# Optimization experiments

Hardware: AMD Instinct MI355X
Metric: run time of the kernel (lower is better)

The kernel has to match this reference:

```python
import jax, jax.numpy as jnp
import numpy as np

H, L, P, D_MODEL = 8, 4, 4, 256
HD = D_MODEL // H
SPATIAL = np.array([[100, 100], [50, 50], [25, 25], [13, 13]], dtype=np.int64)  # (h, w) per level


def _bilinear_sample(feat, gx, gy, lh, lw):
    """Bilinear sampling matching torch.F.grid_sample(align_corners=False, padding_mode='zeros').
    feat: [BH, lh*lw, D]; gx, gy: [BH, Nq, P] pixel coords. Returns [BH, Nq, P, D]."""
    x0 = jnp.floor(gx); y0 = jnp.floor(gy)
    wx = gx - x0; wy = gy - y0

    def gather(xf, yf):
        xi = xf.astype(jnp.int32); yi = yf.astype(jnp.int32)
        valid = (xi >= 0) & (xi < lw) & (yi >= 0) & (yi < lh)
        idx = jnp.clip(yi, 0, lh - 1) * lw + jnp.clip(xi, 0, lw - 1)
        BH = feat.shape[0]
        v = jnp.take_along_axis(feat, idx.reshape(BH, -1)[:, :, None], axis=1)
        v = v.reshape(xi.shape + (feat.shape[-1],))
        return v * valid[..., None].astype(feat.dtype)

    return (gather(x0, y0) * ((1 - wx) * (1 - wy))[..., None]
            + gather(x0 + 1, y0) * (wx * (1 - wy))[..., None]
            + gather(x0, y0 + 1) * ((1 - wx) * wy)[..., None]
            + gather(x0 + 1, y0 + 1) * (wx * wy)[..., None])


def _msda(query, reference_points, value, sp_np, Wso, bso, Waw, baw, Wv, bv, Wo, bo):
    B, Nq, _ = query.shape
    Nv = value.shape[1]
    v = (value @ Wv + bv).reshape(B, Nv, H, HD)  # value_proj
    off = (query @ Wso + bso).reshape(B, Nq, H, L, P, 2)  # sampling_offsets
    wh = jnp.asarray(sp_np[:, ::-1].copy(), jnp.float32)  # (w, h) per level
    loc = reference_points[:, :, None, :, None, :] + off / wh[None, None, None, :, None, :]
    grid = 2.0 * loc - 1.0  # [B, Nq, H, L, P, 2] in [-1, 1]
    aw = jax.nn.softmax((query @ Waw + baw).reshape(B, Nq, H, L * P), axis=-1).reshape(B, Nq, H, L, P)
    starts = np.concatenate([[0], np.cumsum(sp_np[:, 0] * sp_np[:, 1])]).astype(np.int64)
    out = jnp.zeros((B, H, Nq, HD), dtype=query.dtype)
    for lid in range(L):
        lh, lw = int(sp_np[lid, 0]), int(sp_np[lid, 1])
        feat = v[:, starts[lid]:starts[lid + 1]].transpose(0, 2, 1, 3).reshape(B * H, lh * lw, HD)
        g = grid[:, :, :, lid].transpose(0, 2, 1, 3, 4).reshape(B * H, Nq, P, 2)
        # align_corners=False: x_pix = ((gx + 1) * W - 1) / 2
        gx = (g[..., 0] + 1.0) * (lw * 0.5) - 0.5
        gy = (g[..., 1] + 1.0) * (lh * 0.5) - 0.5
        samp = _bilinear_sample(feat, gx, gy, lh, lw)  # [B*H, Nq, P, HD]
        w_l = aw[:, :, :, lid].transpose(0, 2, 1, 3).reshape(B * H, Nq, P)
        out = out + (samp * w_l[..., None]).sum(axis=2).reshape(B, H, Nq, HD)
    out = out.transpose(0, 2, 1, 3).reshape(B, Nq, D_MODEL)
    return out @ Wo + bo  # output_proj


def setup_inputs() -> dict:
    key = jax.random.key(0)
    ks = jax.random.split(key, 12)
    B, Nq = 2, int(np.sum(SPATIAL[:, 0] * SPATIAL[:, 1]))  # encoder: Nq == Nv == 13294
    Nv = Nq
    s = 1.0 / np.sqrt(D_MODEL).astype(np.float32)
    return {
        "query": jax.random.normal(ks[0], (B, Nq, D_MODEL), jnp.float32),
        "reference_points": jax.random.uniform(ks[1], (B, Nq, L, 2), dtype=jnp.float32),
        "value": jax.random.normal(ks[2], (B, Nv, D_MODEL), jnp.float32),
        "spatial_shapes": jnp.asarray(SPATIAL),
        "Wso": jax.random.normal(ks[3], (D_MODEL, H * L * P * 2), jnp.float32) * 0.01,
        "bso": jax.random.normal(ks[4], (H * L * P * 2,), jnp.float32) * 0.5,
        "Waw": jax.random.normal(ks[5], (D_MODEL, H * L * P), jnp.float32) * 0.01,
        "baw": jnp.zeros((H * L * P,), jnp.float32),
        "Wv": jax.random.normal(ks[6], (D_MODEL, D_MODEL), jnp.float32) * s,
        "bv": jnp.zeros((D_MODEL,), jnp.float32),
        "Wo": jax.random.normal(ks[7], (D_MODEL, D_MODEL), jnp.float32) * s,
        "bo": jnp.zeros((D_MODEL,), jnp.float32),
    }


def reference(query, reference_points, value, spatial_shapes, Wso, bso, Waw, baw, Wv, bv, Wo, bo):
    sp_np = np.asarray(spatial_shapes)  # static level shapes
    return _msda(query, reference_points, value, sp_np, Wso, bso, Waw, baw, Wv, bv, Wo, bo)
```

## Files before the change

kernel.cpp:

```cpp
#include <hip/hip_runtime.h>
#include <hip/hip_bf16.h>
#include <hip/hip_fp16.h>

typedef short s16x8 __attribute__((ext_vector_type(8)));
typedef float f32x4 __attribute__((ext_vector_type(4)));
typedef unsigned int u32x4 __attribute__((ext_vector_type(4)));
typedef unsigned int u32x2 __attribute__((ext_vector_type(2)));

constexpr int Bb = 2, NQ = 13294, Hh = 8, HD = 32;
constexpr int Mrows = Bb * NQ;

__device__ inline short bf16_of(float f) {
  __hip_bfloat16 h = __float2bfloat16(f);
  return *reinterpret_cast<short*>(&h);
}

__device__ __forceinline__ void gload16(const void* g, void* l) {
  __builtin_amdgcn_global_load_lds(
      (const __attribute__((address_space(1))) unsigned int*)g,
      (__attribute__((address_space(3))) unsigned int*)l, 16, 0, 0);
}

__global__ __launch_bounds__(256) void prep_k(
    const float* __restrict__ Wv, const float* __restrict__ Wso,
    const float* __restrict__ Waw, const float* __restrict__ Wo,
    const float* __restrict__ bso, const float* __restrict__ baw,
    short* __restrict__ WvT, short* __restrict__ WqT, short* __restrict__ WoT,
    float* __restrict__ bq)
{
  __shared__ short lds[64][65];
  const int tid = threadIdx.x;
  int t = blockIdx.x;
  if (t == 56) {
#pragma unroll
    for (int i = 0; i < 2; i++) {
      int id = i * 256 + tid;
      if (id < 384) bq[id] = id < 256 ? bso[id] : baw[id - 256];
    }
    return;
  }
  const float* src; short* dst; int ldS, n0, k0, drow0;
  if (t < 16)      { src = Wv;  dst = WvT; ldS = 256; n0 = (t >> 2) * 64;        k0 = (t & 3) * 64; drow0 = n0; }
  else if (t < 32) { t -= 16; src = Wso; dst = WqT; ldS = 256; n0 = (t >> 2) * 64; k0 = (t & 3) * 64; drow0 = n0; }
  else if (t < 40) { t -= 32; src = Waw; dst = WqT; ldS = 128; n0 = (t >> 2) * 64; k0 = (t & 3) * 64; drow0 = 256 + n0; }
  else             { t -= 40; src = Wo;  dst = WoT; ldS = 256; n0 = (t >> 2) * 64; k0 = (t & 3) * 64; drow0 = n0; }

#pragma unroll
  for (int i = 0; i < 16; i++) {
    int idx = i * 256 + tid;
    int kk = idx >> 6, nn = idx & 63;
    lds[nn][kk] = bf16_of(src[(size_t)(k0 + kk) * ldS + n0 + nn]);
  }
  __syncthreads();
#pragma unroll
  for (int i = 0; i < 16; i++) {
    int idx = i * 256 + tid;
    int nn = idx >> 6, kk = idx & 63;
    dst[(size_t)(drow0 + nn) * 256 + k0 + kk] = lds[nn][kk];
  }
}

template<int MODE>
__device__ __forceinline__ void gemm_body(
    const void* __restrict__ Araw, const short* __restrict__ WT,
    const float* __restrict__ bias, void* __restrict__ outraw,
    int wg, char* __restrict__ ldsA, char* __restrict__ ldsB)
{
  constexpr int NT = (MODE == 1) ? 3 : 2;
  constexpr int ABYTES = (MODE == 3) ? 8192 : 16384;
  const int xcd = wg & 7, local = wg >> 3;
  const int row0 = (xcd * 26 + local / NT) * 128;
  const int col0 = (local % NT) * 128;
  const int tid = threadIdx.x, lane = tid & 63, wave = tid >> 6;
  const int wr = (wave >> 1) * 64, wc = (wave & 1) * 64;
  const int fr = lane & 15, kg = lane >> 4;

  float bvf[4];
#pragma unroll
  for (int n = 0; n < 4; n++) bvf[n] = bias[col0 + wc + n * 16 + fr];
  asm volatile("" :: "v"(bvf[0]), "v"(bvf[1]), "v"(bvf[2]), "v"(bvf[3]));

  const short* srcB[2]; int ldoffB[2];
#pragma unroll
  for (int i = 0; i < 2; i++) {
    int rowB = i * 64 + (tid >> 2);
    int slB = (tid & 3) ^ ((rowB >> 1) & 3);
    srcB[i] = WT + (size_t)(col0 + rowB) * 256 + slB * 8;
    ldoffB[i] = i * 4096 + tid * 16;
  }
  const float* srcAf[4]; const short* srcAs[2]; int ldoffA[4];
  if constexpr (MODE == 3) {
#pragma unroll
    for (int i = 0; i < 2; i++) {
      int rowA = i * 64 + (tid >> 2);
      int rowc = min(row0 + rowA, Mrows - 1);
      int slA = (tid & 3) ^ ((rowA >> 1) & 3);
      srcAs[i] = (const short*)Araw + (size_t)rowc * 256 + slA * 8;
      ldoffA[i] = i * 4096 + tid * 16;
    }
  } else {
#pragma unroll
    for (int i = 0; i < 4; i++) {
      int rowA = i * 32 + (tid >> 3);
      int rowc = min(row0 + rowA, Mrows - 1);
      int slA = (tid & 7) ^ (rowA & 7);
      srcAf[i] = (const float*)Araw + (size_t)rowc * 256 + slA * 4;
      ldoffA[i] = i * 4096 + tid * 16;
    }
  }

  auto stage = [&](int bufsel, int kt) {
    char* Ab = ldsA + bufsel * ABYTES;
    char* Bd = ldsB + bufsel * 8192;
    if constexpr (MODE == 3) {
#pragma unroll
      for (int i = 0; i < 2; i++) gload16(srcAs[i] + kt, Ab + ldoffA[i]);
    } else {
#pragma unroll
      for (int i = 0; i < 4; i++) gload16(srcAf[i] + kt, Ab + ldoffA[i]);
    }
#pragma unroll
    for (int i = 0; i < 2; i++) gload16(srcB[i] + kt, Bd + ldoffB[i]);
  };

  f32x4 acc[4][4] = {};
  stage(0, 0);

#pragma unroll
  for (int t = 0; t < 8; t++) {
    const int buf = t & 1;
    asm volatile("s_waitcnt vmcnt(0)" ::: "memory");
    __builtin_amdgcn_s_barrier();
    if (t < 7) stage(buf ^ 1, (t + 1) * 32);

    const char* Ab = ldsA + buf * ABYTES;
    const char* Bd = ldsB + buf * 8192;
    s16x8 afr[4], bfr[4];
#pragma unroll
    for (int m = 0; m < 4; m++) {
      const int row = wr + m * 16 + fr;
      if constexpr (MODE == 3) {
        const int slot = kg ^ ((row >> 1) & 3);
        afr[m] = *(const s16x8*)(Ab + row * 64 + slot * 16);
      } else {
        const int s0 = (2 * kg) ^ (row & 7);
        const f32x4 lo = *(const f32x4*)(Ab + row * 128 + s0 * 16);
        const f32x4 hi = *(const f32x4*)(Ab + row * 128 + (s0 ^ 1) * 16);
        s16x8 av;
#pragma unroll
        for (int i = 0; i < 4; i++) { av[i] = bf16_of(lo[i]); av[4 + i] = bf16_of(hi[i]); }
        afr[m] = av;
      }
    }
#pragma unroll
    for (int n = 0; n < 4; n++) {
      const int row = wc + n * 16 + fr;
      const int slot = kg ^ ((row >> 1) & 3);
      bfr[n] = *(const s16x8*)(Bd + row * 64 + slot * 16);
    }
    asm volatile("s_waitcnt lgkmcnt(0)" ::: "memory");

#pragma unroll
    for (int m = 0; m < 4; m++)
#pragma unroll
      for (int n = 0; n < 4; n++)
        acc[m][n] = __builtin_amdgcn_mfma_f32_16x16x32_bf16(afr[m], bfr[n], acc[m][n], 0, 0, 0);
  }

#pragma unroll
  for (int n = 0; n < 4; n++) {
    const int colL = col0 + wc + n * 16 + fr;
#pragma unroll
    for (int m = 0; m < 4; m++) {
#pragma unroll
      for (int r = 0; r < 4; r++) {
        const int rowL = row0 + wr + m * 16 + kg * 4 + r;
        if (rowL < Mrows) {
          float v = acc[m][n][r] + bvf[n];
          if constexpr (MODE == 0) {
            int b = rowL >= NQ, nn = rowL - b * NQ;
            int h = colL >> 5, c = colL & 31;
            ((__half*)outraw)[(((size_t)b * Hh + h) * NQ + nn) * HD + c] = __float2half(v);
          } else if constexpr (MODE == 1) {
            ((__hip_bfloat16*)outraw)[(size_t)rowL * 384 + colL] = __float2bfloat16(v);
          } else {
            ((float*)outraw)[(size_t)rowL * 256 + colL] = v;
          }
        }
      }
    }
  }
}

__global__ __launch_bounds__(256) void gemm01_k(
    const float* __restrict__ value, const float* __restrict__ query,
    const short* __restrict__ WvT, const short* __restrict__ WqT,
    const float* __restrict__ bv, const float* __restrict__ bq,
    __half* __restrict__ vproj, __hip_bfloat16* __restrict__ offaw)
{
  __shared__ __align__(16) char lds[49152];
  char* ldsA = lds;
  char* ldsB = lds + 32768;
  const int wg = blockIdx.x;
  if (wg < 416) gemm_body<0>(value, WvT, bv, vproj, wg, ldsA, ldsB);
  else          gemm_body<1>(query, WqT, bq, offaw, wg - 416, ldsA, ldsB);
}

__global__ __launch_bounds__(256) void gemm3_k(
    const short* __restrict__ interm, const short* __restrict__ WoT,
    const float* __restrict__ bo, float* __restrict__ out)
{
  __shared__ __align__(16) char lds[32768];
  char* ldsA = lds;
  char* ldsB = lds + 16384;
  gemm_body<3>(interm, WoT, bo, out, blockIdx.x, ldsA, ldsB);
}

__global__ __launch_bounds__(256, 8) void sample_k(
    const __half* __restrict__ vproj,
    const __hip_bfloat16* __restrict__ offaw,
    const float* __restrict__ refp,
    __hip_bfloat16* __restrict__ interm)
{
  __shared__ u32x2 dpk[16][2][65];
  const int plane = blockIdx.x & 15;
  const int chunk = blockIdx.x >> 4;
  const int b = plane >> 3, h = plane & 7;
  const int q0 = chunk * 64;
  const int tid = threadIdx.x;
  const int wv = tid >> 6, lane = tid & 63;
  const int dims[4]   = {100, 50, 25, 13};
  const int starts[4] = {0, 10000, 12500, 13125};

#pragma unroll
  for (int it = 0; it < 4; it++) {
    const int ql = wv * 16 + it * 4 + (lane >> 4);
    const int lp = lane & 15;
    const int l = lp >> 2;
    const int lw = dims[l];
    int q = q0 + ql; if (q >= NQ) q = NQ - 1;
    const size_t row = (size_t)b * NQ + q;
    unsigned int oxy = *(const unsigned int*)((const unsigned short*)offaw + row * 384 + h * 32 + lp * 2);
    float offx = __uint_as_float(oxy << 16);
    float offy = __uint_as_float(oxy & 0xffff0000u);
    float logit = __bfloat162float(offaw[row * 384 + 256 + h * 16 + lp]);
    float2 rp = *(const float2*)(refp + (row * 4 + l) * 2);
    float gx = rp.x * (float)lw + offx - 0.5f;
    float gy = rp.y * (float)lw + offy - 0.5f;
    float e = __expf(logit);
    float ssum = e;
#pragma unroll
    for (int d = 1; d < 16; d <<= 1) ssum += __shfl_xor(ssum, d);
    float aw = e / ssum;

    float xf = floorf(gx), yf = floorf(gy);
    int x0 = (int)xf, y0 = (int)yf;
    float wx = gx - xf, wy = gy - yf;
    int bx = min(max(x0, 0), lw - 2);
    bool lxv = (x0 >= 0) & (x0 < lw);
    bool rxv = (x0 + 1 >= 0) & (x0 + 1 < lw);
    float wl = 1.f - wx, wr = wx;
    float ws0 = (lxv && x0 == bx     ? wl : 0.f) + (rxv && x0 + 1 == bx     ? wr : 0.f);
    float ws1 = (lxv && x0 == bx + 1 ? wl : 0.f) + (rxv && x0 + 1 == bx + 1 ? wr : 0.f);
    const int pbase = (b * Hh + h) * NQ + starts[l];
#pragma unroll
    for (int yi = 0; yi < 2; yi++) {
      int yc = y0 + yi;
      bool yv = (yc >= 0) & (yc < lw);
      int ycl = min(max(yc, 0), lw - 1);
      float wyt = (yi ? wy : 1.f - wy) * aw * (yv ? 1.f : 0.f);
      __half h0 = __float2half(ws0 * wyt);
      __half h1 = __float2half(ws1 * wyt);
      u32x2 pk;
      pk[0] = (unsigned int)((pbase + ycl * lw + bx) << 6);
      pk[1] = (unsigned int)(*(unsigned short*)&h0)
            | ((unsigned int)(*(unsigned short*)&h1) << 16);
      dpk[lp][yi][ql] = pk;
    }
  }
  asm volatile("s_waitcnt lgkmcnt(0)" ::: "memory");

  const int qh8 = lane >> 3;
  const int c8  = lane & 7;
  const int shsel = (c8 & 4) << 2;
  const int coff = c8 * 16;
#pragma unroll
  for (int half = 0; half < 2; half++) {
    const int ql = wv * 16 + half * 8 + qh8;
    __half2 acc2[4] = {};
#pragma unroll 4
    for (int lp = 0; lp < 16; lp++) {
#pragma unroll
      for (int yi = 0; yi < 2; yi++) {
        const u32x2 d = dpk[lp][yi][ql];
        const u32x4 u = *(const u32x4*)((const char*)vproj + d[0] + coff);
        unsigned short hw = (unsigned short)((d[1] >> shsel) & 0xffffu);
        __half2 ww = __half2half2(*(const __half*)&hw);
#pragma unroll
        for (int j = 0; j < 4; j++) {
          unsigned int t0 = u[j];
          acc2[j] = __hfma2(*reinterpret_cast<__half2*>(&t0), ww, acc2[j]);
        }
      }
    }
    float2 f[4];
#pragma unroll
    for (int j = 0; j < 4; j++) {
      f[j] = __half22float2(acc2[j]);
      f[j].x += __shfl_xor(f[j].x, 4);
      f[j].y += __shfl_xor(f[j].y, 4);
    }
    const int q = q0 + ql;
    if (c8 < 4 && q < NQ) {
      unsigned int up[4];
#pragma unroll
      for (int j = 0; j < 4; j++) {
        unsigned int b0 = (unsigned int)(unsigned short)bf16_of(f[j].x);
        unsigned int b1 = (unsigned int)(unsigned short)bf16_of(f[j].y);
        up[j] = (b1 << 16) | b0;
      }
      u32x4 pk = { up[0], up[1], up[2], up[3] };
      *(u32x4*)((unsigned short*)interm + ((size_t)b * NQ + q) * 256 + h * 32 + c8 * 8) = pk;
    }
  }
}

extern "C" void kernel_launch(void* const* d_in, const int* in_sizes, int n_in,
                              void* d_out, int out_size, void* d_ws, size_t ws_size,
                              hipStream_t stream)
{
  const float* query = (const float*)d_in[0];
  const float* refp  = (const float*)d_in[1];
  const float* value = (const float*)d_in[2];
  const float* Wso = (const float*)d_in[4];
  const float* bso = (const float*)d_in[5];
  const float* Waw = (const float*)d_in[6];
  const float* baw = (const float*)d_in[7];
  const float* Wv  = (const float*)d_in[8];
  const float* bv  = (const float*)d_in[9];
  const float* Wo  = (const float*)d_in[10];
  const float* bo  = (const float*)d_in[11];

  char* ws = (char*)d_ws;
  __half* vproj          = (__half*)ws;
  __hip_bfloat16* offaw  = (__hip_bfloat16*)(ws + 13613056);
  __hip_bfloat16* interm = (__hip_bfloat16*)(ws + 34032640);
  short* WvT = (short*)(ws + 47645696);
  short* WqT = (short*)(ws + 47776768);
  short* WoT = (short*)(ws + 47973376);
  float* bq  = (float*)(ws + 48104448);
  float* out = (float*)d_out;

  dim3 blk(256);
  prep_k<<<dim3(57), blk, 0, stream>>>(Wv, Wso, Waw, Wo, bso, baw, WvT, WqT, WoT, bq);
  gemm01_k<<<dim3(416 + 624), blk, 0, stream>>>(value, query, WvT, WqT, bv, bq, vproj, offaw);
  sample_k<<<dim3(16 * 208), blk, 0, stream>>>(vproj, offaw, refp, interm);
  gemm3_k<<<dim3(416), blk, 0, stream>>>((const short*)interm, WoT, bo, out);
}
```

Before: 79.29 us.

## Stage fp32 A tiles through registers, convert to bf16 before LDS write

```diff
diff --git a/kernel.cpp b/kernel.cpp
--- a/kernel.cpp
+++ b/kernel.cpp
@@ -3,6 +3,7 @@
 #include <hip/hip_fp16.h>
 
 typedef short s16x8 __attribute__((ext_vector_type(8)));
+typedef short s16x4 __attribute__((ext_vector_type(4)));
 typedef float f32x4 __attribute__((ext_vector_type(4)));
 typedef unsigned int u32x4 __attribute__((ext_vector_type(4)));
 typedef unsigned int u32x2 __attribute__((ext_vector_type(2)));
@@ -67,7 +68,6 @@
     int wg, char* __restrict__ ldsA, char* __restrict__ ldsB)
 {
   constexpr int NT = (MODE == 1) ? 3 : 2;
-  constexpr int ABYTES = (MODE == 3) ? 8192 : 16384;
   const int xcd = wg & 7, local = wg >> 3;
   const int row0 = (xcd * 26 + local / NT) * 128;
   const int col0 = (local % NT) * 128;
@@ -88,7 +88,9 @@
     srcB[i] = WT + (size_t)(col0 + rowB) * 256 + slB * 8;
     ldoffB[i] = i * 4096 + tid * 16;
   }
-  const float* srcAf[4]; const short* srcAs[2]; int ldoffA[4];
+
+  const short* srcAs[2]; int ldoffAs[2];
+  const float* srcAf[4]; int offAw[4];
   if constexpr (MODE == 3) {
 #pragma unroll
     for (int i = 0; i < 2; i++) {
@@ -96,61 +98,70 @@
       int rowc = min(row0 + rowA, Mrows - 1);
       int slA = (tid & 3) ^ ((rowA >> 1) & 3);
       srcAs[i] = (const short*)Araw + (size_t)rowc * 256 + slA * 8;
-      ldoffA[i] = i * 4096 + tid * 16;
+      ldoffAs[i] = i * 4096 + tid * 16;
     }
   } else {
+    const int slot = tid & 7;
 #pragma unroll
     for (int i = 0; i < 4; i++) {
       int rowA = i * 32 + (tid >> 3);
       int rowc = min(row0 + rowA, Mrows - 1);
-      int slA = (tid & 7) ^ (rowA & 7);
-      srcAf[i] = (const float*)Araw + (size_t)rowc * 256 + slA * 4;
-      ldoffA[i] = i * 4096 + tid * 16;
-    }
-  }
-
-  auto stage = [&](int bufsel, int kt) {
-    char* Ab = ldsA + bufsel * ABYTES;
-    char* Bd = ldsB + bufsel * 8192;
+      srcAf[i] = (const float*)Araw + (size_t)rowc * 256 + slot * 4;
+      int cell = (slot >> 1) ^ ((rowA >> 1) & 3);
+      offAw[i] = rowA * 64 + cell * 16 + (slot & 1) * 8;
+    }
+  }
+
+  f32x4 areg[4];
+  auto loadA = [&](int kt) {
+#pragma unroll
+    for (int i = 0; i < 4; i++) areg[i] = *(const f32x4*)(srcAf[i] + kt);
+  };
+  auto writeA = [&](int buf) {
+    char* Ab = ldsA + buf * 8192;
+#pragma unroll
+    for (int i = 0; i < 4; i++) {
+      s16x4 v;
+#pragma unroll
+      for (int j = 0; j < 4; j++) v[j] = bf16_of(areg[i][j]);
+      *(s16x4*)(Ab + offAw[i]) = v;
+    }
+  };
+  auto stageDMA = [&](int buf, int kt) {
+    char* Bd = ldsB + buf * 8192;
+#pragma unroll
+    for (int i = 0; i < 2; i++) gload16(srcB[i] + kt, Bd + ldoffB[i]);
     if constexpr (MODE == 3) {
-#pragma unroll
-      for (int i = 0; i < 2; i++) gload16(srcAs[i] + kt, Ab + ldoffA[i]);
-    } else {
-#pragma unroll
-      for (int i = 0; i < 4; i++) gload16(srcAf[i] + kt, Ab + ldoffA[i]);
-    }
-#pragma unroll
-    for (int i = 0; i < 2; i++) gload16(srcB[i] + kt, Bd + ldoffB[i]);
+      char* Ab = ldsA + buf * 8192;
+#pragma unroll
+      for (int i = 0; i < 2; i++) gload16(srcAs[i] + kt, Ab + ldoffAs[i]);
+    }
   };
 
   f32x4 acc[4][4] = {};
-  stage(0, 0);
+  if constexpr (MODE != 3) loadA(0);
+  stageDMA(0, 0);
 
 #pragma unroll
   for (int t = 0; t < 8; t++) {
     const int buf = t & 1;
     asm volatile("s_waitcnt vmcnt(0)" ::: "memory");
+    if constexpr (MODE != 3) {
+      writeA(buf);
+      if (t < 7) loadA((t + 1) * 32);
+      asm volatile("s_waitcnt lgkmcnt(0)" ::: "memory");
+    }
     __builtin_amdgcn_s_barrier();
-    if (t < 7) stage(buf ^ 1, (t + 1) * 32);
-
-    const char* Ab = ldsA + buf * ABYTES;
+    if (t < 7) stageDMA(buf ^ 1, (t + 1) * 32);
+
+    const char* Ab = ldsA + buf * 8192;
     const char* Bd = ldsB + buf * 8192;
     s16x8 afr[4], bfr[4];
 #pragma unroll
     for (int m = 0; m < 4; m++) {
       const int row = wr + m * 16 + fr;
-      if constexpr (MODE == 3) {
-        const int slot = kg ^ ((row >> 1) & 3);
-        afr[m] = *(const s16x8*)(Ab + row * 64 + slot * 16);
-      } else {
-        const int s0 = (2 * kg) ^ (row & 7);
-        const f32x4 lo = *(const f32x4*)(Ab + row * 128 + s0 * 16);
-        const f32x4 hi = *(const f32x4*)(Ab + row * 128 + (s0 ^ 1) * 16);
-        s16x8 av;
-#pragma unroll
-        for (int i = 0; i < 4; i++) { av[i] = bf16_of(lo[i]); av[4 + i] = bf16_of(hi[i]); }
-        afr[m] = av;
-      }
+      const int slot = kg ^ ((row >> 1) & 3);
+      afr[m] = *(const s16x8*)(Ab + row * 64 + slot * 16);
     }
 #pragma unroll
     for (int n = 0; n < 4; n++) {
@@ -192,21 +203,21 @@
   }
 }
 
-__global__ __launch_bounds__(256) void gemm01_k(
+__global__ __launch_bounds__(256, 5) void gemm01_k(
     const float* __restrict__ value, const float* __restrict__ query,
     const short* __restrict__ WvT, const short* __restrict__ WqT,
     const float* __restrict__ bv, const float* __restrict__ bq,
     __half* __restrict__ vproj, __hip_bfloat16* __restrict__ offaw)
 {
-  __shared__ __align__(16) char lds[49152];
+  __shared__ __align__(16) char lds[32768];
   char* ldsA = lds;
-  char* ldsB = lds + 32768;
+  char* ldsB = lds + 16384;
   const int wg = blockIdx.x;
   if (wg < 416) gemm_body<0>(value, WvT, bv, vproj, wg, ldsA, ldsB);
   else          gemm_body<1>(query, WqT, bq, offaw, wg - 416, ldsA, ldsB);
 }
 
-__global__ __launch_bounds__(256) void gemm3_k(
+__global__ __launch_bounds__(256, 5) void gemm3_k(
     const short* __restrict__ interm, const short* __restrict__ WoT,
     const float* __restrict__ bo, float* __restrict__ out)
 {
```

Result: slower. 169.7 us (+114.1%).
